# Kernel tuning notes

Hardware: AMD Instinct MI355X
Metric: run time of the kernel (lower is better)

Reference implementation:

```python
import jax, jax.numpy as jnp
import numpy as np

N_OBJ = 4096      # n_objects (fixed node count; fc1 consumes flattened node features)
F_IN = 256        # in_feats
H = 256           # n_hidden
C = 128           # n_classes
NE = 8            # number of edge types
EPT = 131072      # edges per etype (avg in-degree 32)


def setup_inputs() -> dict:
    key = jax.random.key(0)
    ks = jax.random.split(key, 16)
    s = 0.02  # weight init scale
    inp = {
        "feat": jax.random.normal(ks[0], (N_OBJ, F_IN), dtype=jnp.float32),
        "edges": jax.random.randint(ks[1], (NE, 2, EPT), 0, N_OBJ, dtype=jnp.int64),
        # 3 hetero layers: layer0 (F_IN->H), layers 1,2 (H->H), each with per-etype Linear
        "W0": jax.random.normal(ks[2], (NE, H, F_IN), dtype=jnp.float32) * s,
        "b0": jnp.zeros((NE, H), dtype=jnp.float32),
        "W1": jax.random.normal(ks[3], (NE, H, H), dtype=jnp.float32) * s,
        "b1": jnp.zeros((NE, H), dtype=jnp.float32),
        "W2": jax.random.normal(ks[4], (NE, H, H), dtype=jnp.float32) * s,
        "b2": jnp.zeros((NE, H), dtype=jnp.float32),
        "fc1_w": jax.random.normal(ks[5], (H, N_OBJ * H), dtype=jnp.float32) * 0.002,
        "fc1_b": jnp.zeros((H,), dtype=jnp.float32),
        "fc2_w": jax.random.normal(ks[6], (C, H), dtype=jnp.float32) * s,
        "fc2_b": jnp.zeros((C,), dtype=jnp.float32),
    }
    return inp


def _hetero_layer(h, W, b, edges):
    # Per-etype linear: Wh[e] = h @ W[e].T + b[e]   -> [NE, N, H]
    Wh = jnp.einsum('nf,ehf->enh', h, W) + b[:, None, :]

    def per_etype(wh, src, dst):
        msg = wh[src]                                            # gather: [EPT, H]
        ssum = jax.ops.segment_sum(msg, dst, num_segments=N_OBJ)  # [N, H]
        deg = jax.ops.segment_sum(jnp.ones_like(dst, dtype=wh.dtype), dst,
                                  num_segments=N_OBJ)             # [N]
        return ssum / jnp.maximum(deg, 1.0)[:, None]              # mean reduce

    agg = jax.vmap(per_etype)(Wh, edges[:, 0], edges[:, 1])  # [NE, N, H]
    # multi_update_all cross-type aggregator 'sum', then activation (relu)
    return jax.nn.relu(agg.sum(axis=0))


def reference(feat, edges, W0, b0, W1, b1, W2, b2, fc1_w, fc1_b, fc2_w, fc2_b):
    h = _hetero_layer(feat, W0, b0, edges)
    h = _hetero_layer(h, W1, b1, edges)
    h = _hetero_layer(h, W2, b2, edges)
    flat = h.reshape(-1)                          # [N*H]
    z = jax.nn.relu(fc1_w @ flat + fc1_b)         # [H]
    out = jax.nn.sigmoid(fc2_w @ z + fc2_b)       # [C]
    return out
```

## Files before the change

### kernel.cpp

```cpp
#include <hip/hip_runtime.h>
#include <math.h>

#define N_OBJ 4096
#define F     256
#define NE    8
#define EPT   131072
#define KCAT  (NE * F)
#define C_OUT 128
#define FC1_K (N_OBJ * F)

typedef __attribute__((ext_vector_type(8))) short s8v;
typedef __attribute__((ext_vector_type(4))) float f4v;

__device__ inline float bf2f(unsigned short u) {
    unsigned int x = ((unsigned int)u) << 16;
    return __builtin_bit_cast(float, x);
}
__device__ inline unsigned short f2bf(float f) {
    unsigned int x = __builtin_bit_cast(unsigned int, f);
    x += 0x7fff + ((x >> 16) & 1);
    return (unsigned short)(x >> 16);
}


__global__ __launch_bounds__(256) void k_count_deg(const int* __restrict__ edges,
                                                   int* __restrict__ deg) {
    int gid = blockIdx.x * 256 + threadIdx.x;
    int e = gid >> 17;
    int i = gid & (EPT - 1);
    int dst = edges[(e * 2 + 1) * EPT + i];
    atomicAdd(&deg[e * N_OBJ + dst], 1);
}

__global__ __launch_bounds__(256) void k_scan(const int* __restrict__ deg,
                                              int* __restrict__ rowptr,
                                              int* __restrict__ cursor,
                                              float* __restrict__ invdeg) {
    int e = blockIdx.x;
    int t = threadIdx.x;
    __shared__ int part[256];
    int local[16];
    int base = e * N_OBJ + t * 16;
    int s = 0;
#pragma unroll
    for (int i = 0; i < 16; ++i) { local[i] = deg[base + i]; s += local[i]; }
    part[t] = s;
    __syncthreads();
    for (int off = 1; off < 256; off <<= 1) {
        int v = (t >= off) ? part[t - off] : 0;
        __syncthreads();
        part[t] += v;
        __syncthreads();
    }
    int run = part[t] - s;
#pragma unroll
    for (int i = 0; i < 16; ++i) {
        rowptr[base + i] = run;
        cursor[base + i] = run;
        invdeg[base + i] = 1.0f / fmaxf((float)local[i], 1.0f);
        run += local[i];
    }
}

__global__ __launch_bounds__(256) void k_fill(const int* __restrict__ edges,
                                              int* __restrict__ cursor,
                                              int* __restrict__ col) {
    int gid = blockIdx.x * 256 + threadIdx.x;
    int e = gid >> 17;
    int i = gid & (EPT - 1);
    int src = edges[(e * 2 + 0) * EPT + i];
    int dst = edges[(e * 2 + 1) * EPT + i];
    int pos = atomicAdd(&cursor[e * N_OBJ + dst], 1);
    col[e * EPT + pos] = src;
}

__global__ __launch_bounds__(256) void k_bmask(const int* __restrict__ deg,
                                               unsigned int* __restrict__ bmask) {
    int n = blockIdx.x * 256 + threadIdx.x;
    unsigned int m = 0;
#pragma unroll
    for (int e = 0; e < NE; ++e) m |= (deg[e * N_OBJ + n] > 0) ? (1u << e) : 0u;
    bmask[n] = m;
}

__global__ __launch_bounds__(256) void k_cvt(const float* __restrict__ s,
                                             unsigned short* __restrict__ d, int n4) {
    int i = blockIdx.x * 256 + threadIdx.x;
    if (i < n4) {
        float4 v = ((const float4*)s)[i];
        ushort4 o;
        o.x = f2bf(v.x); o.y = f2bf(v.y); o.z = f2bf(v.z); o.w = f2bf(v.w);
        ((ushort4*)d)[i] = o;
    }
}

template <int INBF>
__global__ __launch_bounds__(64) void k_aggregate(const void* __restrict__ h_in,
                                                  const int* __restrict__ rowptr,
                                                  const int* __restrict__ deg,
                                                  const int* __restrict__ col,
                                                  const float* __restrict__ invdeg,
                                                  unsigned short* __restrict__ ah) {
    int bid = blockIdx.x;
    int e = bid >> 12;
    int n = bid & (N_OBJ - 1);
    int lane = threadIdx.x;
    int idx = e * N_OBJ + n;
    int beg = rowptr[idx];
    int cnt = deg[idx];
    const int* cl = col + e * EPT + beg;
    float a0 = 0.f, a1 = 0.f, a2 = 0.f, a3 = 0.f;
    int k = 0;
    if (INBF) {
        const ushort4* h4 = (const ushort4*)h_in;
        for (; k + 4 <= cnt; k += 4) {
            int s0 = cl[k], s1 = cl[k + 1], s2 = cl[k + 2], s3 = cl[k + 3];
            ushort4 v0 = h4[s0 * 64 + lane];
            ushort4 v1 = h4[s1 * 64 + lane];
            ushort4 v2 = h4[s2 * 64 + lane];
            ushort4 v3 = h4[s3 * 64 + lane];
            a0 += bf2f(v0.x) + bf2f(v1.x) + bf2f(v2.x) + bf2f(v3.x);
            a1 += bf2f(v0.y) + bf2f(v1.y) + bf2f(v2.y) + bf2f(v3.y);
            a2 += bf2f(v0.z) + bf2f(v1.z) + bf2f(v2.z) + bf2f(v3.z);
            a3 += bf2f(v0.w) + bf2f(v1.w) + bf2f(v2.w) + bf2f(v3.w);
        }
        for (; k < cnt; ++k) {
            ushort4 v = h4[cl[k] * 64 + lane];
            a0 += bf2f(v.x); a1 += bf2f(v.y); a2 += bf2f(v.z); a3 += bf2f(v.w);
        }
    } else {
        const float4* h4 = (const float4*)h_in;
        for (; k + 4 <= cnt; k += 4) {
            int s0 = cl[k], s1 = cl[k + 1], s2 = cl[k + 2], s3 = cl[k + 3];
            float4 v0 = h4[s0 * 64 + lane];
            float4 v1 = h4[s1 * 64 + lane];
            float4 v2 = h4[s2 * 64 + lane];
            float4 v3 = h4[s3 * 64 + lane];
            a0 += v0.x + v1.x + v2.x + v3.x;
            a1 += v0.y + v1.y + v2.y + v3.y;
            a2 += v0.z + v1.z + v2.z + v3.z;
            a3 += v0.w + v1.w + v2.w + v3.w;
        }
        for (; k < cnt; ++k) {
            float4 v = h4[cl[k] * 64 + lane];
            a0 += v.x; a1 += v.y; a2 += v.z; a3 += v.w;
        }
    }
    float sc = invdeg[idx];
    ushort4 o;
    o.x = f2bf(a0 * sc); o.y = f2bf(a1 * sc); o.z = f2bf(a2 * sc); o.w = f2bf(a3 * sc);
    ((ushort4*)ah)[n * (KCAT / 4) + e * (F / 4) + lane] = o;
}

template <int OUTBF>
__global__ __launch_bounds__(256) void k_gemm(const unsigned short* __restrict__ A,
                                              const unsigned short* __restrict__ Wb,
                                              const float* __restrict__ bias,
                                              const unsigned int* __restrict__ bmask,
                                              void* __restrict__ Cout) {
    __shared__ short As[64][40];
    __shared__ short Bs[64][40];
    int m0 = blockIdx.x * 64, n0 = blockIdx.y * 64;
    int t = threadIdx.x;
    int wave = t >> 6, lane = t & 63;
    int srow = t >> 2, sseg = t & 3;
    int r = lane & 15, g = lane >> 4;
    f4v acc[4];
#pragma unroll
    for (int i = 0; i < 4; ++i) acc[i] = (f4v){0.f, 0.f, 0.f, 0.f};
    const short* Ap = (const short*)A;
    const short* Wp = (const short*)Wb;
    for (int k0 = 0; k0 < KCAT; k0 += 32) {
        int e = k0 >> 8, f0 = k0 & 255;
        s8v va = *(const s8v*)(Ap + (size_t)(m0 + srow) * KCAT + k0 + sseg * 8);
        s8v vb = *(const s8v*)(Wp + (size_t)e * F * F + (size_t)(n0 + srow) * F + f0 + sseg * 8);
        __syncthreads();
        *(s8v*)&As[srow][sseg * 8] = va;
        *(s8v*)&Bs[srow][sseg * 8] = vb;
        __syncthreads();
        s8v bfrag = *(const s8v*)&Bs[wave * 16 + r][g * 8];
#pragma unroll
        for (int mf = 0; mf < 4; ++mf) {
            s8v afrag = *(const s8v*)&As[mf * 16 + r][g * 8];
            acc[mf] = __builtin_amdgcn_mfma_f32_16x16x32_bf16(afrag, bfrag, acc[mf], 0, 0, 0);
        }
    }
    int coln = n0 + wave * 16 + r;
    float bcol[NE];
#pragma unroll
    for (int e = 0; e < NE; ++e) bcol[e] = bias[e * F + coln];
#pragma unroll
    for (int mf = 0; mf < 4; ++mf) {
#pragma unroll
        for (int reg = 0; reg < 4; ++reg) {
            int m = m0 + mf * 16 + g * 4 + reg;
            unsigned int msk = bmask[m];
            float v = acc[mf][reg];
#pragma unroll
            for (int e = 0; e < NE; ++e)
                if ((msk >> e) & 1) v += bcol[e];
            v = fmaxf(v, 0.f);
            if (OUTBF) ((unsigned short*)Cout)[(size_t)m * F + coln] = f2bf(v);
            else       ((float*)Cout)[(size_t)m * F + coln] = v;
        }
    }
}

__global__ __launch_bounds__(256) void k_fc1(const float* __restrict__ Wf,
                                             const float* __restrict__ flat,
                                             float* __restrict__ zpart) {
    int c = blockIdx.x;
    int j = blockIdx.y;
    int t = threadIdx.x;
    const float4* wp = (const float4*)(Wf + (size_t)j * FC1_K + (size_t)c * 65536);
    const float4* fp = (const float4*)(flat + (size_t)c * 65536);
    float s = 0.0f;
#pragma unroll 4
    for (int it = 0; it < 64; ++it) {
        int q = it * 256 + t;
        float4 w4 = wp[q];
        float4 x4 = fp[q];
        s = fmaf(w4.x, x4.x, s);
        s = fmaf(w4.y, x4.y, s);
        s = fmaf(w4.z, x4.z, s);
        s = fmaf(w4.w, x4.w, s);
    }
#pragma unroll
    for (int off = 32; off > 0; off >>= 1) s += __shfl_down(s, off, 64);
    __shared__ float red[4];
    if ((t & 63) == 0) red[t >> 6] = s;
    __syncthreads();
    if (t == 0) zpart[c * 256 + j] = red[0] + red[1] + red[2] + red[3];
}

__global__ __launch_bounds__(256) void k_final(const float* __restrict__ zpart,
                                               const float* __restrict__ fc1_b,
                                               const float* __restrict__ fc2_w,
                                               const float* __restrict__ fc2_b,
                                               float* __restrict__ out) {
    __shared__ float z[256];
    int t = threadIdx.x;
    float s = fc1_b[t];
#pragma unroll
    for (int c = 0; c < 16; ++c) s += zpart[c * 256 + t];
    z[t] = fmaxf(s, 0.0f);
    __syncthreads();
    if (t < C_OUT) {
        float acc = fc2_b[t];
        for (int k = 0; k < 256; ++k) acc = fmaf(fc2_w[t * 256 + k], z[k], acc);
        out[t] = 1.0f / (1.0f + expf(-acc));
    }
}

extern "C" void kernel_launch(void* const* d_in, const int* in_sizes, int n_in,
                              void* d_out, int out_size, void* d_ws, size_t ws_size,
                              hipStream_t stream) {
    const float* feat  = (const float*)d_in[0];
    const int*   edges = (const int*)d_in[1];
    const float* W0    = (const float*)d_in[2];
    const float* b0    = (const float*)d_in[3];
    const float* W1    = (const float*)d_in[4];
    const float* b1    = (const float*)d_in[5];
    const float* W2    = (const float*)d_in[6];
    const float* b2    = (const float*)d_in[7];
    const float* fc1_w = (const float*)d_in[8];
    const float* fc1_b = (const float*)d_in[9];
    const float* fc2_w = (const float*)d_in[10];
    const float* fc2_b = (const float*)d_in[11];
    float* out = (float*)d_out;

    char* ws = (char*)d_ws;
    size_t off = 0;
    auto alloc = [&](size_t bytes) {
        void* p = ws + off;
        off = (off + bytes + 255) & ~(size_t)255;
        return p;
    };
    int*            deg    = (int*)            alloc(NE * N_OBJ * 4);
    int*            rowptr = (int*)            alloc(NE * N_OBJ * 4);
    int*            cursor = (int*)            alloc(NE * N_OBJ * 4);
    float*          invdeg = (float*)          alloc(NE * N_OBJ * 4);
    int*            col    = (int*)            alloc(NE * EPT * 4);
    unsigned int*   bmask  = (unsigned int*)   alloc(N_OBJ * 4);
    float*          zpart  = (float*)          alloc(16 * 256 * 4);
    unsigned short* Wb0    = (unsigned short*) alloc((size_t)NE * F * F * 2);
    unsigned short* Wb1    = (unsigned short*) alloc((size_t)NE * F * F * 2);
    unsigned short* Wb2    = (unsigned short*) alloc((size_t)NE * F * F * 2);
    unsigned short* h_ba   = (unsigned short*) alloc((size_t)N_OBJ * F * 2);
    unsigned short* h_bb   = (unsigned short*) alloc((size_t)N_OBJ * F * 2);
    float*          h_f32  = (float*)          alloc((size_t)N_OBJ * F * 4);
    unsigned short* ah     = (unsigned short*) alloc((size_t)N_OBJ * KCAT * 2);
    (void)ws_size; (void)in_sizes; (void)n_in; (void)out_size;

    hipMemsetAsync(deg, 0, NE * N_OBJ * 4, stream);
    k_count_deg<<<NE * EPT / 256, 256, 0, stream>>>(edges, deg);
    k_scan<<<NE, 256, 0, stream>>>(deg, rowptr, cursor, invdeg);
    k_fill<<<NE * EPT / 256, 256, 0, stream>>>(edges, cursor, col);
    k_bmask<<<N_OBJ / 256, 256, 0, stream>>>(deg, bmask);
    k_cvt<<<512, 256, 0, stream>>>(W0, Wb0, NE * F * F / 4);
    k_cvt<<<512, 256, 0, stream>>>(W1, Wb1, NE * F * F / 4);
    k_cvt<<<512, 256, 0, stream>>>(W2, Wb2, NE * F * F / 4);

    dim3 ggrid(N_OBJ / 64, F / 64);

    k_aggregate<0><<<NE * N_OBJ, 64, 0, stream>>>(feat, rowptr, deg, col, invdeg, ah);
    k_gemm<1><<<ggrid, 256, 0, stream>>>(ah, Wb0, b0, bmask, h_ba);
    k_aggregate<1><<<NE * N_OBJ, 64, 0, stream>>>(h_ba, rowptr, deg, col, invdeg, ah);
    k_gemm<1><<<ggrid, 256, 0, stream>>>(ah, Wb1, b1, bmask, h_bb);
    k_aggregate<1><<<NE * N_OBJ, 64, 0, stream>>>(h_bb, rowptr, deg, col, invdeg, ah);
    k_gemm<0><<<ggrid, 256, 0, stream>>>(ah, Wb2, b2, bmask, h_f32);

    dim3 fgrid(16, 256);
    k_fc1<<<fgrid, 256, 0, stream>>>(fc1_w, h_f32, zpart);
    k_final<<<1, 256, 0, stream>>>(zpart, fc1_b, fc2_w, fc2_b, out);
}
```

Baseline: 501.0 us.

## Convert features to bf16, pack aggregate waves per block, register-block fc1 rows

Input features are converted to bf16 first, so the first aggregation gathers half the bytes and one bf16 aggregate kernel serves all layers. The aggregate kernel now packs four node-waves per 256-thread block and unrolls the gather by 8 for more memory-level parallelism. fc1 computes 8 output rows per block over 32K-element chunks, reusing each loaded flat vector across rows to cut redundant reads of the activations. This adds one conversion pass and rounds the first layer's input to bf16, which costs some precision.

Result: slower. 522.9 us (+4.4%).

```diff
diff --git a/kernel.cpp b/kernel.cpp
--- a/kernel.cpp
+++ b/kernel.cpp
@@ -8,6 +8,9 @@
 #define KCAT  (NE * F)
 #define C_OUT 128
 #define FC1_K (N_OBJ * F)
+#define CHUNK 32768
+#define NCH   (FC1_K / CHUNK)
+#define RPB   8
 
 typedef __attribute__((ext_vector_type(8))) short s8v;
 typedef __attribute__((ext_vector_type(4))) float f4v;
@@ -94,59 +97,47 @@
     }
 }
 
-template <int INBF>
-__global__ __launch_bounds__(64) void k_aggregate(const void* __restrict__ h_in,
-                                                  const int* __restrict__ rowptr,
-                                                  const int* __restrict__ deg,
-                                                  const int* __restrict__ col,
-                                                  const float* __restrict__ invdeg,
-                                                  unsigned short* __restrict__ ah) {
-    int bid = blockIdx.x;
-    int e = bid >> 12;
-    int n = bid & (N_OBJ - 1);
-    int lane = threadIdx.x;
-    int idx = e * N_OBJ + n;
-    int beg = rowptr[idx];
-    int cnt = deg[idx];
+__global__ __launch_bounds__(256) void k_aggregate(const unsigned short* __restrict__ h_in,
+                                                   const int* __restrict__ rowptr,
+                                                   const int* __restrict__ deg,
+                                                   const int* __restrict__ col,
+                                                   const float* __restrict__ invdeg,
+                                                   unsigned short* __restrict__ ah) {
+    int wid = blockIdx.x * 4 + (threadIdx.x >> 6);
+    int lane = threadIdx.x & 63;
+    int e = wid >> 12;
+    int n = wid & (N_OBJ - 1);
+    int beg = rowptr[wid];
+    int cnt = deg[wid];
     const int* cl = col + e * EPT + beg;
+    const ushort4* h4 = (const ushort4*)h_in;
     float a0 = 0.f, a1 = 0.f, a2 = 0.f, a3 = 0.f;
     int k = 0;
-    if (INBF) {
-        const ushort4* h4 = (const ushort4*)h_in;
-        for (; k + 4 <= cnt; k += 4) {
-            int s0 = cl[k], s1 = cl[k + 1], s2 = cl[k + 2], s3 = cl[k + 3];
-            ushort4 v0 = h4[s0 * 64 + lane];
-            ushort4 v1 = h4[s1 * 64 + lane];
-            ushort4 v2 = h4[s2 * 64 + lane];
-            ushort4 v3 = h4[s3 * 64 + lane];
-            a0 += bf2f(v0.x) + bf2f(v1.x) + bf2f(v2.x) + bf2f(v3.x);
-            a1 += bf2f(v0.y) + bf2f(v1.y) + bf2f(v2.y) + bf2f(v3.y);
-            a2 += bf2f(v0.z) + bf2f(v1.z) + bf2f(v2.z) + bf2f(v3.z);
-            a3 += bf2f(v0.w) + bf2f(v1.w) + bf2f(v2.w) + bf2f(v3.w);
-        }
-        for (; k < cnt; ++k) {
-            ushort4 v = h4[cl[k] * 64 + lane];
-            a0 += bf2f(v.x); a1 += bf2f(v.y); a2 += bf2f(v.z); a3 += bf2f(v.w);
-        }
-    } else {
-        const float4* h4 = (const float4*)h_in;
-        for (; k + 4 <= cnt; k += 4) {
-            int s0 = cl[k], s1 = cl[k + 1], s2 = cl[k + 2], s3 = cl[k + 3];
-            float4 v0 = h4[s0 * 64 + lane];
-            float4 v1 = h4[s1 * 64 + lane];
-            float4 v2 = h4[s2 * 64 + lane];
-            float4 v3 = h4[s3 * 64 + lane];
-            a0 += v0.x + v1.x + v2.x + v3.x;
-            a1 += v0.y + v1.y + v2.y + v3.y;
-            a2 += v0.z + v1.z + v2.z + v3.z;
-            a3 += v0.w + v1.w + v2.w + v3.w;
-        }
-        for (; k < cnt; ++k) {
-            float4 v = h4[cl[k] * 64 + lane];
-            a0 += v.x; a1 += v.y; a2 += v.z; a3 += v.w;
-        }
-    }
-    float sc = invdeg[idx];
+    for (; k + 8 <= cnt; k += 8) {
+        int s0 = cl[k],     s1 = cl[k + 1], s2 = cl[k + 2], s3 = cl[k + 3];
+        int s4 = cl[k + 4], s5 = cl[k + 5], s6 = cl[k + 6], s7 = cl[k + 7];
+        ushort4 v0 = h4[s0 * 64 + lane];
+        ushort4 v1 = h4[s1 * 64 + lane];
+        ushort4 v2 = h4[s2 * 64 + lane];
+        ushort4 v3 = h4[s3 * 64 + lane];
+        ushort4 v4 = h4[s4 * 64 + lane];
+        ushort4 v5 = h4[s5 * 64 + lane];
+        ushort4 v6 = h4[s6 * 64 + lane];
+        ushort4 v7 = h4[s7 * 64 + lane];
+        a0 += bf2f(v0.x) + bf2f(v1.x) + bf2f(v2.x) + bf2f(v3.x)
+            + bf2f(v4.x) + bf2f(v5.x) + bf2f(v6.x) + bf2f(v7.x);
+        a1 += bf2f(v0.y) + bf2f(v1.y) + bf2f(v2.y) + bf2f(v3.y)
+            + bf2f(v4.y) + bf2f(v5.y) + bf2f(v6.y) + bf2f(v7.y);
+        a2 += bf2f(v0.z) + bf2f(v1.z) + bf2f(v2.z) + bf2f(v3.z)
+            + bf2f(v4.z) + bf2f(v5.z) + bf2f(v6.z) + bf2f(v7.z);
+        a3 += bf2f(v0.w) + bf2f(v1.w) + bf2f(v2.w) + bf2f(v3.w)
+            + bf2f(v4.w) + bf2f(v5.w) + bf2f(v6.w) + bf2f(v7.w);
+    }
+    for (; k < cnt; ++k) {
+        ushort4 v = h4[cl[k] * 64 + lane];
+        a0 += bf2f(v.x); a1 += bf2f(v.y); a2 += bf2f(v.z); a3 += bf2f(v.w);
+    }
+    float sc = invdeg[wid];
     ushort4 o;
     o.x = f2bf(a0 * sc); o.y = f2bf(a1 * sc); o.z = f2bf(a2 * sc); o.w = f2bf(a3 * sc);
     ((ushort4*)ah)[n * (KCAT / 4) + e * (F / 4) + lane] = o;
@@ -210,27 +201,38 @@
                                              const float* __restrict__ flat,
                                              float* __restrict__ zpart) {
     int c = blockIdx.x;
-    int j = blockIdx.y;
+    int jg = blockIdx.y;
     int t = threadIdx.x;
-    const float4* wp = (const float4*)(Wf + (size_t)j * FC1_K + (size_t)c * 65536);
-    const float4* fp = (const float4*)(flat + (size_t)c * 65536);
-    float s = 0.0f;
-#pragma unroll 4
-    for (int it = 0; it < 64; ++it) {
+    const float4* fp = (const float4*)(flat + (size_t)c * CHUNK);
+    size_t base = (size_t)(jg * RPB) * FC1_K + (size_t)c * CHUNK;
+    float acc[RPB] = {};
+#pragma unroll 2
+    for (int it = 0; it < CHUNK / 4 / 256; ++it) {
         int q = it * 256 + t;
-        float4 w4 = wp[q];
         float4 x4 = fp[q];
-        s = fmaf(w4.x, x4.x, s);
-        s = fmaf(w4.y, x4.y, s);
-        s = fmaf(w4.z, x4.z, s);
-        s = fmaf(w4.w, x4.w, s);
-    }
-#pragma unroll
-    for (int off = 32; off > 0; off >>= 1) s += __shfl_down(s, off, 64);
-    __shared__ float red[4];
-    if ((t & 63) == 0) red[t >> 6] = s;
+#pragma unroll
+        for (int rr = 0; rr < RPB; ++rr) {
+            float4 w4 = *(const float4*)(Wf + base + (size_t)rr * FC1_K + (size_t)q * 4);
+            acc[rr] = fmaf(w4.x, x4.x,
+                      fmaf(w4.y, x4.y,
+                      fmaf(w4.z, x4.z,
+                      fmaf(w4.w, x4.w, acc[rr]))));
+        }
+    }
+    __shared__ float red[4][RPB];
+    int lane = t & 63, wv = t >> 6;
+#pragma unroll
+    for (int rr = 0; rr < RPB; ++rr) {
+        float s = acc[rr];
+#pragma unroll
+        for (int off = 32; off > 0; off >>= 1) s += __shfl_down(s, off, 64);
+        if (lane == 0) red[wv][rr] = s;
+    }
     __syncthreads();
-    if (t == 0) zpart[c * 256 + j] = red[0] + red[1] + red[2] + red[3];
+    if (t < RPB) {
+        float s = red[0][t] + red[1][t] + red[2][t] + red[3][t];
+        zpart[c * 256 + jg * RPB + t] = s;
+    }
 }
 
 __global__ __launch_bounds__(256) void k_final(const float* __restrict__ zpart,
@@ -242,7 +244,7 @@
     int t = threadIdx.x;
     float s = fc1_b[t];
 #pragma unroll
-    for (int c = 0; c < 16; ++c) s += zpart[c * 256 + t];
+    for (int c = 0; c < NCH; ++c) s += zpart[c * 256 + t];
     z[t] = fmaxf(s, 0.0f);
     __syncthreads();
     if (t < C_OUT) {
@@ -282,10 +284,11 @@
     float*          invdeg = (float*)          alloc(NE * N_OBJ * 4);
     int*            col    = (int*)            alloc(NE * EPT * 4);
     unsigned int*   bmask  = (unsigned int*)   alloc(N_OBJ * 4);
-    float*          zpart  = (float*)          alloc(16 * 256 * 4);
+    float*          zpart  = (float*)          alloc(NCH * 256 * 4);
     unsigned short* Wb0    = (unsigned short*) alloc((size_t)NE * F * F * 2);
     unsigned short* Wb1    = (unsigned short*) alloc((size_t)NE * F * F * 2);
     unsigned short* Wb2    = (unsigned short*) alloc((size_t)NE * F * F * 2);
+    unsigned short* featb  = (unsigned short*) alloc((size_t)N_OBJ * F * 2);
     unsigned short* h_ba   = (unsigned short*) alloc((size_t)N_OBJ * F * 2);
     unsigned short* h_bb   = (unsigned short*) alloc((size_t)N_OBJ * F * 2);
     float*          h_f32  = (float*)          alloc((size_t)N_OBJ * F * 4);
@@ -300,17 +303,19 @@
     k_cvt<<<512, 256, 0, stream>>>(W0, Wb0, NE * F * F / 4);
     k_cvt<<<512, 256, 0, stream>>>(W1, Wb1, NE * F * F / 4);
     k_cvt<<<512, 256, 0, stream>>>(W2, Wb2, NE * F * F / 4);
+    k_cvt<<<1024, 256, 0, stream>>>(feat, featb, N_OBJ * F / 4);
 
     dim3 ggrid(N_OBJ / 64, F / 64);
-
-    k_aggregate<0><<<NE * N_OBJ, 64, 0, stream>>>(feat, rowptr, deg, col, invdeg, ah);
+    int agrid = NE * N_OBJ / 4;
+
+    k_aggregate<<<agrid, 256, 0, stream>>>(featb, rowptr, deg, col, invdeg, ah);
     k_gemm<1><<<ggrid, 256, 0, stream>>>(ah, Wb0, b0, bmask, h_ba);
-    k_aggregate<1><<<NE * N_OBJ, 64, 0, stream>>>(h_ba, rowptr, deg, col, invdeg, ah);
+    k_aggregate<<<agrid, 256, 0, stream>>>(h_ba, rowptr, deg, col, invdeg, ah);
     k_gemm<1><<<ggrid, 256, 0, stream>>>(ah, Wb1, b1, bmask, h_bb);
-    k_aggregate<1><<<NE * N_OBJ, 64, 0, stream>>>(h_bb, rowptr, deg, col, invdeg, ah);
+    k_aggregate<<<agrid, 256, 0, stream>>>(h_bb, rowptr, deg, col, invdeg, ah);
     k_gemm<0><<<ggrid, 256, 0, stream>>>(ah, Wb2, b2, bmask, h_f32);
 
-    dim3 fgrid(16, 256);
+    dim3 fgrid(NCH, 256 / RPB);
     k_fc1<<<fgrid, 256, 0, stream>>>(fc1_w, h_f32, zpart);
     k_final<<<1, 256, 0, stream>>>(zpart, fc1_b, fc2_w, fc2_b, out);
 }
```
